# Kernel tuning notes

Measured on AMD Instinct MI355X. Metric: run time of the kernel, lower is better.

## Reference

```python
import jax, jax.numpy as jnp
import numpy as np

B, N, D, DEPTH = 1, 512, 128, 4


def mlp_apply(W, x):
    # W: (depth, d, d), x: (..., d). First layer has no activation, then silu before each matmul.
    x = x @ W[0]
    for i in range(1, DEPTH):
        x = jax.nn.silu(x) @ W[i]
    return x


def _binop(x, y):
    # linear recurrence combine: s_t = a_t * s_{t-1} + b_t
    a1, b1 = x
    a2, b2 = y
    return (a1 * a2, a2 * b1 + b2)


def setup_inputs() -> dict:
    key = jax.random.key(0)
    ks = jax.random.split(key, 7)
    s = 0.02  # scale for projection weights (torch Linear-like init magnitude)
    return {
        "seq": jax.random.normal(ks[0], (B, N, D), jnp.float32),
        "W_mem": jax.random.normal(ks[1], (DEPTH, D, D), jnp.float32) * (D ** -0.5),
        "W_q": jax.random.normal(ks[2], (D, D), jnp.float32) * s,
        "W_kv": jax.random.normal(ks[3], (D, 2 * D), jnp.float32) * s,
        "W_mom": jax.random.normal(ks[4], (D, 1), jnp.float32) * s,
        "W_step": jax.random.normal(ks[5], (D, 1), jnp.float32) * s,
        "W_decay": jax.random.normal(ks[6], (D, 1), jnp.float32) * s,
    }


def reference(seq, W_mem, W_q, W_kv, W_mom, W_step, W_decay):
    b, n, d = seq.shape
    # --- store_memories ---
    adaptive_lr = (seq @ W_step)[..., 0]            # (b, n)
    adaptive_mom = seq @ W_mom                      # (b, n, 1)
    decay = jax.nn.sigmoid(seq @ W_decay)           # (b, n, 1)

    kv = seq.reshape(b * n, d) @ W_kv               # (bn, 2d)
    keys, values = kv[:, :d], kv[:, d:]

    def loss_fn(W, k, v):
        pred = mlp_apply(W, k)                      # (d,)
        # (pred - v)^2 .mean(-1).sum() for a single sample == mean over d
        return jnp.mean((pred - v) ** 2)

    # per-sample meta-gradients wrt memory MLP weights
    losses, grads = jax.vmap(jax.value_and_grad(loss_fn, argnums=0), in_axes=(None, 0, 0))(W_mem, keys, values)
    grads = grads.reshape(b, n, DEPTH, d, d)
    surprise = grads * (-adaptive_lr)[..., None, None, None]   # (b,n,depth,d,d)

    # momentum_t = adaptive_mom_t * momentum_{t-1} + surprise_t  (assoc. scan over n)
    am = adaptive_mom[..., None, None]              # (b, n, 1, 1, 1)
    _, momentum = jax.lax.associative_scan(_binop, (am, surprise), axis=1)

    # update_t = (1 - decay_t) * update_{t-1} + momentum_t
    dec = (1.0 - decay)[..., None, None]            # (b, n, 1, 1, 1)
    _, updates = jax.lax.associative_scan(_binop, (dec, momentum), axis=1)

    # --- retrieve_memories with per-token updated weights ---
    q = (seq @ W_q).reshape(b * n, d)
    W_tok = (W_mem[None, None] + updates).reshape(b * n, DEPTH, d, d)
    retrieved = jax.vmap(mlp_apply)(W_tok, q).reshape(b, n, d)
    return retrieved
```

## Files before the change

### kernel.cpp

```cpp
#include <hip/hip_runtime.h>
#include <hip/hip_bf16.h>
#include <math.h>

#define N 512
#define NN (N*N)
#define D 128
#define DD (D*D)
#define ND (N*D)
#define LSTR 132
#define CSTR 68

__device__ __forceinline__ float sigmoidf_(float x) { return 1.f / (1.f + expf(-x)); }

__global__ void k_transpose(const float* __restrict__ W_mem, float* __restrict__ WT) {
    int idx = blockIdx.x * 256 + threadIdx.x;
    int l = idx / DD;
    int r = idx % DD;
    int i = r / D;
    int j = r % D;
    WT[idx] = W_mem[(l + 1) * DD + j * D + i];
}

__global__ __launch_bounds__(512) void k_phase1(
    const float* __restrict__ seq, const float* __restrict__ W_mem,
    const float* __restrict__ W_q, const float* __restrict__ W_kv,
    const float* __restrict__ W_mom, const float* __restrict__ W_step,
    const float* __restrict__ W_decay, const float* __restrict__ WT,
    float* __restrict__ Q, float* __restrict__ INS, float* __restrict__ ES,
    float* __restrict__ am, float* __restrict__ dec)
{
    __shared__ float s_seq[4][D];
    __shared__ float s_bufA[4][D];
    __shared__ float s_bufB[4][D];
    __shared__ float s_red[4][2][3];
    __shared__ float s_lr[4];

    const int tid = threadIdx.x;
    const int tok = tid >> 7;
    const int j   = tid & 127;
    const int t   = blockIdx.x * 4 + tok;

    float sv = seq[t * D + j];
    s_seq[tok][j] = sv;

    float p0 = sv * W_step[j];
    float p1 = sv * W_mom[j];
    float p2 = sv * W_decay[j];
#pragma unroll
    for (int off = 32; off > 0; off >>= 1) {
        p0 += __shfl_down(p0, off);
        p1 += __shfl_down(p1, off);
        p2 += __shfl_down(p2, off);
    }
    if ((tid & 63) == 0) {
        int w = (tid >> 6) & 1;
        s_red[tok][w][0] = p0;
        s_red[tok][w][1] = p1;
        s_red[tok][w][2] = p2;
    }
    __syncthreads();
    if (j == 0) {
        s_lr[tok] = s_red[tok][0][0] + s_red[tok][1][0];
        am[t]     = s_red[tok][0][1] + s_red[tok][1][1];
        dec[t]    = 1.f - sigmoidf_(s_red[tok][0][2] + s_red[tok][1][2]);
    }

    float kj = 0.f, vj = 0.f, qj = 0.f;
    {
        const float* sq = s_seq[tok];
#pragma unroll 8
        for (int i = 0; i < D; i++) {
            float si = sq[i];
            kj += si * W_kv[i * 256 + j];
            vj += si * W_kv[i * 256 + 128 + j];
            qj += si * W_q[i * 128 + j];
        }
    }
    Q[t * D + j] = qj;
    INS[t * D + j] = kj;
    s_bufA[tok][j] = kj;
    __syncthreads();

    float hreg[4];
    float pred = 0.f;
    {
        float* curs[2] = { &s_bufA[0][0], &s_bufB[0][0] };
        for (int l = 0; l < 4; l++) {
            const float* cur = curs[l & 1] + tok * D;
            float* nxt = curs[(l + 1) & 1] + tok * D;
            const float* Wp = W_mem + l * DD + j;
            float a0 = 0.f, a1 = 0.f, a2 = 0.f, a3 = 0.f;
#pragma unroll 8
            for (int i = 0; i < D; i += 4) {
                a0 += cur[i]     * Wp[i * D];
                a1 += cur[i + 1] * Wp[(i + 1) * D];
                a2 += cur[i + 2] * Wp[(i + 2) * D];
                a3 += cur[i + 3] * Wp[(i + 3) * D];
            }
            float y = (a0 + a1) + (a2 + a3);
            hreg[l] = y;
            if (l < 3) {
                float a = y * sigmoidf_(y);
                nxt[j] = a;
                INS[(l + 1) * ND + t * D + j] = a;
            } else {
                pred = y;
            }
            __syncthreads();
        }

        float e = -s_lr[tok] * (2.f / (float)D) * (pred - vj);
        ES[3 * ND + t * D + j] = e;
        curs[0][tok * D + j] = e;
        __syncthreads();

        for (int l = 3; l >= 1; l--) {
            const float* cur = curs[(3 - l) & 1] + tok * D;
            float* nxt = curs[(3 - l + 1) & 1] + tok * D;
            const float* Wp = WT + (l - 1) * DD + j;
            float a0 = 0.f, a1 = 0.f, a2 = 0.f, a3 = 0.f;
#pragma unroll 8
            for (int i = 0; i < D; i += 4) {
                a0 += cur[i]     * Wp[i * D];
                a1 += cur[i + 1] * Wp[(i + 1) * D];
                a2 += cur[i + 2] * Wp[(i + 2) * D];
                a3 += cur[i + 3] * Wp[(i + 3) * D];
            }
            float g = (a0 + a1) + (a2 + a3);
            float h = hreg[l - 1];
            float sg = sigmoidf_(h);
            float e2 = g * (sg * (1.f + h * (1.f - sg)));
            ES[(l - 1) * ND + t * D + j] = e2;
            nxt[j] = e2;
            __syncthreads();
        }
    }
}

__global__ __launch_bounds__(512) void k_logscan(
    const float* __restrict__ am, const float* __restrict__ dec,
    double* __restrict__ LA, double* __restrict__ LDp, int* __restrict__ NC)
{
    __shared__ double sa[N], sd[N];
    __shared__ int sn[N];
    const int t = threadIdx.x;
    float a = am[t];
    float d = dec[t];
    sa[t] = log((double)fmaxf(fabsf(a), 1e-38f));
    sd[t] = log((double)fmaxf(d, 1e-38f));
    sn[t] = (a < 0.f) ? 1 : 0;
    __syncthreads();
    for (int off = 1; off < N; off <<= 1) {
        double va = 0.0, vd = 0.0; int vn = 0;
        if (t >= off) { va = sa[t - off]; vd = sd[t - off]; vn = sn[t - off]; }
        __syncthreads();
        sa[t] += va; sd[t] += vd; sn[t] += vn;
        __syncthreads();
    }
    LA[t] = sa[t]; LDp[t] = sd[t]; NC[t] = sn[t];
}

__global__ __launch_bounds__(256) void k_build(
    const double* __restrict__ LA, const double* __restrict__ LDp,
    const int* __restrict__ NC,
    float* __restrict__ Amat, float* __restrict__ Dmat)
{
    int idx = blockIdx.x * 256 + threadIdx.x;
    int u = idx >> 9;
    int s = idx & (N - 1);
    float va = 0.f, vd = 0.f;
    if (s <= u) {
        va = expf((float)(LA[u] - LA[s]));
        if ((NC[u] - NC[s]) & 1) va = -va;
        vd = expf((float)(LDp[u] - LDp[s]));
    }
    Amat[idx] = va;
    Dmat[idx] = vd;
}

__global__ __launch_bounds__(256) void k_betamm(
    const float* __restrict__ Dmat, const float* __restrict__ Amat,
    float* __restrict__ betaP)
{
    const int bs = blockIdx.x;
    const int bt = blockIdx.y;
    const int z  = blockIdx.z;
    if (bs > bt) return;
    const int span = bt - bs + 1;
    const int chunk = (span + 3) >> 2;
    const int kBeg = bs + z * chunk;
    const int kEnd = (kBeg + chunk < bt + 1) ? (kBeg + chunk) : (bt + 1);
    if (kBeg >= kEnd) return;

    __shared__ float sA[32 * 34];
    __shared__ float sDT[32 * 34];

    const int tid = threadIdx.x;
    const int tx = tid & 15;
    const int ty = tid >> 4;
    float acc00 = 0.f, acc01 = 0.f, acc10 = 0.f, acc11 = 0.f;

    for (int kt = kBeg; kt < kEnd; kt++) {
        for (int i = tid; i < 1024; i += 256) {
            int r = i >> 5, c = i & 31;
            sA[r * 34 + c]  = Amat[(kt * 32 + r) * N + bs * 32 + c];
            sDT[c * 34 + r] = Dmat[(bt * 32 + r) * N + kt * 32 + c];
        }
        __syncthreads();
#pragma unroll 8
        for (int k = 0; k < 32; k++) {
            float2 a = *(float2*)&sA[k * 34 + 2 * tx];
            float2 d = *(float2*)&sDT[k * 34 + 2 * ty];
            acc00 += d.x * a.x; acc01 += d.x * a.y;
            acc10 += d.y * a.x; acc11 += d.y * a.y;
        }
        __syncthreads();
    }
    float* bp = betaP + z * NN + (bt * 32 + 2 * ty) * N + bs * 32 + 2 * tx;
    *(float2*)bp       = make_float2(acc00, acc01);
    *(float2*)(bp + N) = make_float2(acc10, acc11);
}

__global__ __launch_bounds__(256) void k_betared(
    const float* __restrict__ betaP, float* __restrict__ beta)
{
    int idx4 = blockIdx.x * 256 + threadIdx.x;
    int t  = idx4 >> 7;
    int s0 = (idx4 & 127) * 4;
    int bt = t >> 5, bs = s0 >> 5;
    float4 v = make_float4(0.f, 0.f, 0.f, 0.f);
    if (bs <= bt) {
        int span = bt - bs + 1;
        int chunk = (span + 3) >> 2;
        int nz = (span + chunk - 1) / chunk;
        v = *(const float4*)(betaP + t * N + s0);
        for (int z = 1; z < nz; z++) {
            float4 u = *(const float4*)(betaP + z * NN + t * N + s0);
            v.x += u.x; v.y += u.y; v.z += u.z; v.w += u.w;
        }
    }
    *(float4*)(beta + t * N + s0) = v;
}

__global__ __launch_bounds__(256) void k_layer(
    const float* __restrict__ Xsrc, float* __restrict__ Pout,
    const float* __restrict__ Wl, const float* __restrict__ INSl,
    const float* __restrict__ ESl, const float* __restrict__ beta,
    int mode)
{
    const int r = blockIdx.x;
    const int z = blockIdx.y;
    const bool isW = (z == 8);
    if (!isW && 4 * z > r) return;
    const int t0 = r * 16;
    const int lane = threadIdx.x;

    __shared__ __align__(16) float sX[16 * LSTR];
    __shared__ __align__(16) float sI[64 * LSTR];
    __shared__ __align__(16) float sE[32 * LSTR];
    __shared__ __align__(16) float sc[16 * CSTR];

    const int nzs = (r >> 2) + 1;
#pragma unroll
    for (int i = 0; i < 2; i++) {
        int f4 = lane + 256 * i;
        int row = f4 >> 5, c4 = f4 & 31;
        float4 v = ((const float4*)(Xsrc + t0 * D))[f4];
        if (mode) {
            for (int zz = 1; zz < nzs; zz++) {
                float4 u = ((const float4*)(Xsrc + zz * ND + t0 * D))[f4];
                v.x += u.x; v.y += u.y; v.z += u.z; v.w += u.w;
            }
            float4 w = ((const float4*)(Xsrc + 8 * ND + t0 * D))[f4];
            v.x += w.x; v.y += w.y; v.z += w.z; v.w += w.w;
            v.x = v.x * sigmoidf_(v.x); v.y = v.y * sigmoidf_(v.y);
            v.z = v.z * sigmoidf_(v.z); v.w = v.w * sigmoidf_(v.w);
        }
        *(float4*)(sX + row * LSTR + c4 * 4) = v;
    }

    if (isW) {
        __syncthreads();
        const int ti  = lane >> 4;
        const int j8  = (lane & 15) * 8;
        float acc[8];
#pragma unroll
        for (int b = 0; b < 8; b++) acc[b] = 0.f;
#pragma unroll 4
        for (int k = 0; k < D; k++) {
            float4 w0 = *(const float4*)(Wl + k * D + j8);
            float4 w1 = *(const float4*)(Wl + k * D + j8 + 4);
            float xv = sX[ti * LSTR + k];
            acc[0] += xv * w0.x; acc[1] += xv * w0.y;
            acc[2] += xv * w0.z; acc[3] += xv * w0.w;
            acc[4] += xv * w1.x; acc[5] += xv * w1.y;
            acc[6] += xv * w1.z; acc[7] += xv * w1.w;
        }
        float* yp = Pout + 8 * ND + (t0 + ti) * D + j8;
        *(float4*)yp       = make_float4(acc[0], acc[1], acc[2], acc[3]);
        *(float4*)(yp + 4) = make_float4(acc[4], acc[5], acc[6], acc[7]);
        return;
    }

    const int s0 = z * 64;
#pragma unroll
    for (int i = 0; i < 8; i++) {
        int f4 = lane + 256 * i;
        int row = f4 >> 5, c4 = f4 & 31;
        float4 a = ((const float4*)(INSl + s0 * D))[f4];
        *(float4*)(sI + row * LSTR + c4 * 4) = a;
    }

    const int rp = lane >> 5;
    const int sp = lane & 31;
    float b00 = beta[(t0 + 2 * rp) * N + s0 + sp];
    float b01 = beta[(t0 + 2 * rp) * N + s0 + sp + 32];
    float b10 = beta[(t0 + 2 * rp + 1) * N + s0 + sp];
    float b11 = beta[(t0 + 2 * rp + 1) * N + s0 + sp + 32];
    __syncthreads();

    float g00 = 0.f, g01 = 0.f, g10 = 0.f, g11 = 0.f;
#pragma unroll 8
    for (int k4 = 0; k4 < D; k4 += 4) {
        float4 a0 = *(float4*)(sX + (2 * rp) * LSTR + k4);
        float4 a1 = *(float4*)(sX + (2 * rp + 1) * LSTR + k4);
        float4 p0 = *(float4*)(sI + sp * LSTR + k4);
        float4 p1 = *(float4*)(sI + (sp + 32) * LSTR + k4);
        g00 += a0.x * p0.x + a0.y * p0.y + a0.z * p0.z + a0.w * p0.w;
        g01 += a0.x * p1.x + a0.y * p1.y + a0.z * p1.z + a0.w * p1.w;
        g10 += a1.x * p0.x + a1.y * p0.y + a1.z * p0.z + a1.w * p0.w;
        g11 += a1.x * p1.x + a1.y * p1.y + a1.z * p1.z + a1.w * p1.w;
    }
    sc[(2 * rp) * CSTR + sp]          = g00 * b00;
    sc[(2 * rp) * CSTR + sp + 32]     = g01 * b01;
    sc[(2 * rp + 1) * CSTR + sp]      = g10 * b10;
    sc[(2 * rp + 1) * CSTR + sp + 32] = g11 * b11;

    const int tp = lane >> 5;
    const int jc = (lane & 31) * 4;
    float acc[2][4];
#pragma unroll
    for (int a = 0; a < 2; a++)
#pragma unroll
        for (int b = 0; b < 4; b++) acc[a][b] = 0.f;

    for (int sub = 0; sub < 2; sub++) {
        __syncthreads();
#pragma unroll
        for (int i = 0; i < 4; i++) {
            int f4 = lane + 256 * i;
            int row = f4 >> 5, c4 = f4 & 31;
            float4 b = ((const float4*)(ESl + (s0 + sub * 32) * D))[f4];
            *(float4*)(sE + row * LSTR + c4 * 4) = b;
        }
        __syncthreads();
        const float* scp0 = sc + tp * CSTR + sub * 32;
        const float* scp1 = sc + (tp + 8) * CSTR + sub * 32;
#pragma unroll 8
        for (int s = 0; s < 32; s++) {
            float c0 = scp0[s];
            float c1 = scp1[s];
            float4 e = *(float4*)(sE + s * LSTR + jc);
            acc[0][0] += c0 * e.x; acc[0][1] += c0 * e.y;
            acc[0][2] += c0 * e.z; acc[0][3] += c0 * e.w;
            acc[1][0] += c1 * e.x; acc[1][1] += c1 * e.y;
            acc[1][2] += c1 * e.z; acc[1][3] += c1 * e.w;
        }
    }

    float* yp0 = Pout + z * ND + (t0 + tp) * D + jc;
    float* yp1 = Pout + z * ND + (t0 + tp + 8) * D + jc;
    *(float4*)yp0 = make_float4(acc[0][0], acc[0][1], acc[0][2], acc[0][3]);
    *(float4*)yp1 = make_float4(acc[1][0], acc[1][1], acc[1][2], acc[1][3]);
}

__global__ __launch_bounds__(256) void k_reduce(
    const float* __restrict__ P, float* __restrict__ out)
{
    int f4 = blockIdx.x * 256 + threadIdx.x;
    int t = f4 >> 5;
    int r = t >> 4;
    int nzs = (r >> 2) + 1;
    float4 v = ((const float4*)P)[f4];
    for (int zz = 1; zz < nzs; zz++) {
        float4 u = ((const float4*)(P + zz * ND))[f4];
        v.x += u.x; v.y += u.y; v.z += u.z; v.w += u.w;
    }
    float4 w = ((const float4*)(P + 8 * ND))[f4];
    v.x += w.x; v.y += w.y; v.z += w.z; v.w += w.w;
    ((float4*)out)[f4] = v;
}

extern "C" void kernel_launch(void* const* d_in, const int* in_sizes, int n_in,
                              void* d_out, int out_size, void* d_ws, size_t ws_size,
                              hipStream_t stream) {
    const float* seq     = (const float*)d_in[0];
    const float* W_mem   = (const float*)d_in[1];
    const float* W_q     = (const float*)d_in[2];
    const float* W_kv    = (const float*)d_in[3];
    const float* W_mom   = (const float*)d_in[4];
    const float* W_step  = (const float*)d_in[5];
    const float* W_decay = (const float*)d_in[6];
    float* out = (float*)d_out;

    float* ws   = (float*)d_ws;
    float* am   = ws;
    float* dec  = am + N;
    float* Q    = dec + N;
    float* INS  = Q + ND;
    float* ES   = INS + 4 * ND;
    float* beta = ES + 4 * ND;
    float* WT   = beta + NN;
    float* Amat = WT + 3 * DD;
    float* Dmat = Amat + NN;
    float* Pa   = Dmat + NN;
    float* Pb   = Pa + 9 * ND;
    double* LA  = (double*)(Pb + 9 * ND);
    double* LDp = LA + N;
    int* NC     = (int*)(LDp + N);
    float* betaP = Pa;

    k_transpose<<<192, 256, 0, stream>>>(W_mem, WT);
    k_phase1<<<N / 4, 512, 0, stream>>>(seq, W_mem, W_q, W_kv, W_mom, W_step, W_decay,
                                        WT, Q, INS, ES, am, dec);
    k_logscan<<<1, N, 0, stream>>>(am, dec, LA, LDp, NC);
    k_build<<<(NN) / 256, 256, 0, stream>>>(LA, LDp, NC, Amat, Dmat);
    dim3 mmgrid(N / 32, N / 32, 4);
    k_betamm<<<mmgrid, 256, 0, stream>>>(Dmat, Amat, betaP);
    k_betared<<<NN / 4 / 256, 256, 0, stream>>>(betaP, beta);

    dim3 lgrid(32, 9);
    k_layer<<<lgrid, 256, 0, stream>>>(Q,  Pa, W_mem,          INS,          ES,          beta, 0);
    k_layer<<<lgrid, 256, 0, stream>>>(Pa, Pb, W_mem + DD,     INS + ND,     ES + ND,     beta, 1);
    k_layer<<<lgrid, 256, 0, stream>>>(Pb, Pa, W_mem + 2 * DD, INS + 2 * ND, ES + 2 * ND, beta, 1);
    k_layer<<<lgrid, 256, 0, stream>>>(Pa, Pb, W_mem + 3 * DD, INS + 3 * ND, ES + 3 * ND, beta, 1);
    k_reduce<<<64, 256, 0, stream>>>(Pb, out);
}
```

Measured before the change: 172.5 us.

## Split phase1 reduction dimension across thread groups with two tokens per block

```diff
diff --git a/kernel.cpp b/kernel.cpp
--- a/kernel.cpp
+++ b/kernel.cpp
@@ -29,109 +29,146 @@
     float* __restrict__ Q, float* __restrict__ INS, float* __restrict__ ES,
     float* __restrict__ am, float* __restrict__ dec)
 {
-    __shared__ float s_seq[4][D];
-    __shared__ float s_bufA[4][D];
-    __shared__ float s_bufB[4][D];
-    __shared__ float s_red[4][2][3];
-    __shared__ float s_lr[4];
+    __shared__ float s_seq[2][D];
+    __shared__ float s_bufA[2][D];
+    __shared__ float s_bufB[2][D];
+    __shared__ float s_p3[4][2][3][D];
+    __shared__ float s_part[4][2][D];
+    __shared__ float s_red8[8][3];
+    __shared__ float s_lr[2];
 
     const int tid = threadIdx.x;
-    const int tok = tid >> 7;
+    const int p   = tid >> 7;
     const int j   = tid & 127;
-    const int t   = blockIdx.x * 4 + tok;
-
-    float sv = seq[t * D + j];
-    s_seq[tok][j] = sv;
-
-    float p0 = sv * W_step[j];
-    float p1 = sv * W_mom[j];
-    float p2 = sv * W_decay[j];
-#pragma unroll
-    for (int off = 32; off > 0; off >>= 1) {
-        p0 += __shfl_down(p0, off);
-        p1 += __shfl_down(p1, off);
-        p2 += __shfl_down(p2, off);
-    }
-    if ((tid & 63) == 0) {
-        int w = (tid >> 6) & 1;
-        s_red[tok][w][0] = p0;
-        s_red[tok][w][1] = p1;
-        s_red[tok][w][2] = p2;
-    }
-    __syncthreads();
-    if (j == 0) {
-        s_lr[tok] = s_red[tok][0][0] + s_red[tok][1][0];
-        am[t]     = s_red[tok][0][1] + s_red[tok][1][1];
-        dec[t]    = 1.f - sigmoidf_(s_red[tok][0][2] + s_red[tok][1][2]);
-    }
-
-    float kj = 0.f, vj = 0.f, qj = 0.f;
+    const int t0  = blockIdx.x * 2;
+    const int i0  = p * 32;
+
+    if (p < 2) s_seq[p][j] = seq[(t0 + p) * D + j];
+    __syncthreads();
+
     {
-        const float* sq = s_seq[tok];
-#pragma unroll 8
-        for (int i = 0; i < D; i++) {
-            float si = sq[i];
-            kj += si * W_kv[i * 256 + j];
-            vj += si * W_kv[i * 256 + 128 + j];
-            qj += si * W_q[i * 128 + j];
-        }
-    }
-    Q[t * D + j] = qj;
-    INS[t * D + j] = kj;
-    s_bufA[tok][j] = kj;
+        const int wv   = tid >> 6;
+        const int tok  = wv >> 2;
+        const int half = (wv >> 1) & 1;
+        float sv = s_seq[tok][j];
+        float p0 = 0.f, p1 = 0.f, p2 = 0.f;
+        if (half == 0) { p0 = sv * W_step[j]; p1 = sv * W_mom[j]; }
+        else           { p2 = sv * W_decay[j]; }
+#pragma unroll
+        for (int off = 32; off > 0; off >>= 1) {
+            p0 += __shfl_down(p0, off);
+            p1 += __shfl_down(p1, off);
+            p2 += __shfl_down(p2, off);
+        }
+        if ((tid & 63) == 0) {
+            s_red8[wv][0] = p0; s_red8[wv][1] = p1; s_red8[wv][2] = p2;
+        }
+    }
+    __syncthreads();
+    if (tid < 2) {
+        int b = tid * 4;
+        s_lr[tid]  = s_red8[b][0] + s_red8[b + 1][0];
+        am[t0+tid] = s_red8[b][1] + s_red8[b + 1][1];
+        dec[t0+tid]= 1.f - sigmoidf_(s_red8[b + 2][2] + s_red8[b + 3][2]);
+    }
+
+    float k0 = 0.f, v0 = 0.f, q0 = 0.f;
+    float k1 = 0.f, v1 = 0.f, q1 = 0.f;
+#pragma unroll 8
+    for (int ii = 0; ii < 32; ii++) {
+        int i = i0 + ii;
+        float wk = W_kv[i * 256 + j];
+        float wq = W_q[i * 128 + j];
+        float wvv = W_kv[i * 256 + 128 + j];
+        float a0 = s_seq[0][i], a1 = s_seq[1][i];
+        k0 += a0 * wk;  k1 += a1 * wk;
+        v0 += a0 * wvv; v1 += a1 * wvv;
+        q0 += a0 * wq;  q1 += a1 * wq;
+    }
+    s_p3[p][0][0][j] = k0; s_p3[p][0][1][j] = v0; s_p3[p][0][2][j] = q0;
+    s_p3[p][1][0][j] = k1; s_p3[p][1][1][j] = v1; s_p3[p][1][2][j] = q1;
+    __syncthreads();
+
+    float vj = 0.f;
+    if (p < 2) {
+        const int tok = p;
+        float kj = s_p3[0][tok][0][j] + s_p3[1][tok][0][j] + s_p3[2][tok][0][j] + s_p3[3][tok][0][j];
+        vj       = s_p3[0][tok][1][j] + s_p3[1][tok][1][j] + s_p3[2][tok][1][j] + s_p3[3][tok][1][j];
+        float qj = s_p3[0][tok][2][j] + s_p3[1][tok][2][j] + s_p3[2][tok][2][j] + s_p3[3][tok][2][j];
+        Q[(t0 + tok) * D + j] = qj;
+        INS[(t0 + tok) * D + j] = kj;
+        s_bufA[tok][j] = kj;
+    }
     __syncthreads();
 
     float hreg[4];
     float pred = 0.f;
     {
-        float* curs[2] = { &s_bufA[0][0], &s_bufB[0][0] };
+        float (*bufs[2])[D] = { s_bufA, s_bufB };
         for (int l = 0; l < 4; l++) {
-            const float* cur = curs[l & 1] + tok * D;
-            float* nxt = curs[(l + 1) & 1] + tok * D;
+            float (*cur)[D] = bufs[l & 1];
+            float (*nxt)[D] = bufs[(l + 1) & 1];
             const float* Wp = W_mem + l * DD + j;
-            float a0 = 0.f, a1 = 0.f, a2 = 0.f, a3 = 0.f;
-#pragma unroll 8
-            for (int i = 0; i < D; i += 4) {
-                a0 += cur[i]     * Wp[i * D];
-                a1 += cur[i + 1] * Wp[(i + 1) * D];
-                a2 += cur[i + 2] * Wp[(i + 2) * D];
-                a3 += cur[i + 3] * Wp[(i + 3) * D];
+            float a0 = 0.f, a1 = 0.f;
+#pragma unroll 8
+            for (int ii = 0; ii < 32; ii++) {
+                int i = i0 + ii;
+                float w = Wp[i * D];
+                a0 += cur[0][i] * w;
+                a1 += cur[1][i] * w;
             }
-            float y = (a0 + a1) + (a2 + a3);
-            hreg[l] = y;
-            if (l < 3) {
-                float a = y * sigmoidf_(y);
-                nxt[j] = a;
-                INS[(l + 1) * ND + t * D + j] = a;
-            } else {
-                pred = y;
+            s_part[p][0][j] = a0;
+            s_part[p][1][j] = a1;
+            __syncthreads();
+            if (p < 2) {
+                const int tok = p;
+                float y = (s_part[0][tok][j] + s_part[1][tok][j])
+                        + (s_part[2][tok][j] + s_part[3][tok][j]);
+                hreg[l] = y;
+                if (l < 3) {
+                    float a = y * sigmoidf_(y);
+                    nxt[tok][j] = a;
+                    INS[(l + 1) * ND + (t0 + tok) * D + j] = a;
+                } else {
+                    pred = y;
+                }
             }
             __syncthreads();
         }
 
-        float e = -s_lr[tok] * (2.f / (float)D) * (pred - vj);
-        ES[3 * ND + t * D + j] = e;
-        curs[0][tok * D + j] = e;
+        if (p < 2) {
+            const int tok = p;
+            float e = -s_lr[tok] * (2.f / (float)D) * (pred - vj);
+            ES[3 * ND + (t0 + tok) * D + j] = e;
+            bufs[0][tok][j] = e;
+        }
         __syncthreads();
 
         for (int l = 3; l >= 1; l--) {
-            const float* cur = curs[(3 - l) & 1] + tok * D;
-            float* nxt = curs[(3 - l + 1) & 1] + tok * D;
+            float (*cur)[D] = bufs[(3 - l) & 1];
+            float (*nxt)[D] = bufs[(3 - l + 1) & 1];
             const float* Wp = WT + (l - 1) * DD + j;
-            float a0 = 0.f, a1 = 0.f, a2 = 0.f, a3 = 0.f;
-#pragma unroll 8
-            for (int i = 0; i < D; i += 4) {
-                a0 += cur[i]     * Wp[i * D];
-                a1 += cur[i + 1] * Wp[(i + 1) * D];
-                a2 += cur[i + 2] * Wp[(i + 2) * D];
-                a3 += cur[i + 3] * Wp[(i + 3) * D];
+            float a0 = 0.f, a1 = 0.f;
+#pragma unroll 8
+            for (int ii = 0; ii < 32; ii++) {
+                int i = i0 + ii;
+                float w = Wp[i * D];
+                a0 += cur[0][i] * w;
+                a1 += cur[1][i] * w;
             }
-            float g = (a0 + a1) + (a2 + a3);
-            float h = hreg[l - 1];
-            float sg = sigmoidf_(h);
-            float e2 = g * (sg * (1.f + h * (1.f - sg)));
-            ES[(l - 1) * ND + t * D + j] = e2;
-            nxt[j] = e2;
+            s_part[p][0][j] = a0;
+            s_part[p][1][j] = a1;
+            __syncthreads();
+            if (p < 2) {
+                const int tok = p;
+                float g = (s_part[0][tok][j] + s_part[1][tok][j])
+                        + (s_part[2][tok][j] + s_part[3][tok][j]);
+                float h = hreg[l - 1];
+                float sg = sigmoidf_(h);
+                float e2 = g * (sg * (1.f + h * (1.f - sg)));
+                ES[(l - 1) * ND + (t0 + tok) * D + j] = e2;
+                nxt[tok][j] = e2;
+            }
             __syncthreads();
         }
     }
@@ -421,7 +458,7 @@
     float* betaP = Pa;
 
     k_transpose<<<192, 256, 0, stream>>>(W_mem, WT);
-    k_phase1<<<N / 4, 512, 0, stream>>>(seq, W_mem, W_q, W_kv, W_mom, W_step, W_decay,
+    k_phase1<<<N / 2, 512, 0, stream>>>(seq, W_mem, W_q, W_kv, W_mom, W_step, W_decay,
                                         WT, Q, INS, ES, am, dec);
     k_logscan<<<1, N, 0, stream>>>(am, dec, LA, LDp, NC);
     k_build<<<(NN) / 256, 256, 0, stream>>>(LA, LDp, NC, Amat, Dmat);
```

New measurement: 163.5 us. 1.05x faster.
